# Performance work log

Hardware: AMD Instinct MI355X
Metric: run time of the kernel (lower is better)

## Reference

```python
import jax, jax.numpy as jnp
import numpy as np
from jax import lax

K = 9
CENTER = K // 2
EXTEND = 1.0
EPS = 1e-5
GROUPS = 16  # out_ch // 4


def conv2d(x, w, b, stride, padding):
    y = lax.conv_general_dilated(x, w, window_strides=stride, padding=padding,
                                 dimension_numbers=('NCHW', 'OIHW', 'NCHW'))
    return y + b[None, :, None, None]


def setup_inputs() -> dict:
    key = jax.random.key(0)
    ks = jax.random.split(key, 9)
    B, C, Wd, Hd, OUT = 8, 64, 128, 128, 64
    f = jax.random.normal(ks[0], (B, C, Wd, Hd), jnp.float32)
    w_off = jax.random.normal(ks[1], (2 * K, C, 3, 3), jnp.float32) * 0.05
    b_off = jax.random.normal(ks[2], (2 * K,), jnp.float32) * 0.05
    bn_gamma = 1.0 + 0.1 * jax.random.normal(ks[3], (2 * K,), jnp.float32)
    bn_beta = 0.1 * jax.random.normal(ks[4], (2 * K,), jnp.float32)
    w_dsc = jax.random.normal(ks[5], (OUT, C, K, 1), jnp.float32) * 0.05
    b_dsc = jax.random.normal(ks[6], (OUT,), jnp.float32) * 0.05
    gn_gamma = 1.0 + 0.1 * jax.random.normal(ks[7], (OUT,), jnp.float32)
    gn_beta = 0.1 * jax.random.normal(ks[8], (OUT,), jnp.float32)
    return {'f': f, 'w_off': w_off, 'b_off': b_off, 'bn_gamma': bn_gamma,
            'bn_beta': bn_beta, 'w_dsc': w_dsc, 'b_dsc': b_dsc,
            'gn_gamma': gn_gamma, 'gn_beta': gn_beta}


def _forward(f, w_off, b_off, bn_gamma, bn_beta, w_dsc, b_dsc, gn_gamma, gn_beta):
    B, C, Wd, Hd = f.shape  # module names: width=shape[2], height=shape[3]
    dt = f.dtype

    # offset branch: conv3x3 -> BatchNorm (training mode, batch stats) -> tanh
    off = conv2d(f, w_off, b_off, (1, 1), 'SAME')
    mu = off.mean(axis=(0, 2, 3), keepdims=True)
    var = off.var(axis=(0, 2, 3), keepdims=True)
    off = (off - mu) / jnp.sqrt(var + EPS)
    off = off * bn_gamma[None, :, None, None] + bn_beta[None, :, None, None]
    off = jnp.tanh(off)

    y_off = off[:, :K]  # [B,K,Wd,Hd]; x_off (off[:, K:]) unused for morph=0

    # cumulative offset scan from the center point (morph=0).
    # NOTE: endpoints 0 and K-1 keep detached raw offsets (torch detach().clone()).
    raw0 = lax.stop_gradient(y_off)
    offn = [None] * K
    offn[CENTER] = jnp.zeros_like(y_off[:, 0])
    for i in range(1, CENTER):
        offn[CENTER + i] = offn[CENTER + i - 1] + y_off[:, CENTER + i]
        offn[CENTER - i] = offn[CENTER - i + 1] + y_off[:, CENTER - i]
    offn[0] = raw0[:, 0]
    offn[K - 1] = raw0[:, K - 1]
    offn = jnp.stack(offn, axis=1)  # [B,K,Wd,Hd]

    # coordinate grids: y indexes the width axis, x the height axis
    y_new = jnp.arange(Wd, dtype=dt)[None, None, :, None] + offn * EXTEND  # [B,K,Wd,Hd]
    x_new = ((jnp.arange(K, dtype=dt) - CENTER)[None, :, None, None]
             + jnp.arange(Hd, dtype=dt)[None, None, None, :])  # [1,K,1,Hd]
    x_new = jnp.broadcast_to(x_new, (B, K, Wd, Hd))

    # layout [B, K*Wd, Hd] via (B,K,Wd,Hd) -> (B,Wd,K,Hd)
    y_s = jnp.transpose(y_new, (0, 2, 1, 3)).reshape(B, K * Wd * Hd)
    x_s = jnp.transpose(x_new, (0, 2, 1, 3)).reshape(B, K * Wd * Hd)

    # bilinear interpolation (clamped corner indices, unclamped y/x in weights)
    y0 = jnp.floor(y_s).astype(jnp.int32)
    x0 = jnp.floor(x_s).astype(jnp.int32)
    y0c = jnp.clip(y0, 0, Wd - 1)
    y1c = jnp.clip(y0 + 1, 0, Wd - 1)
    x0c = jnp.clip(x0, 0, Hd - 1)
    x1c = jnp.clip(x0 + 1, 0, Hd - 1)

    feat = jnp.transpose(f, (0, 2, 3, 1)).reshape(B, Wd * Hd, C)

    def gather(yi, xi):
        idx = (yi * Hd + xi)[:, :, None]  # [B,N,1]
        return jnp.take_along_axis(feat, idx, axis=1)  # [B,N,C]

    va0 = gather(y0c, x0c)
    vc0 = gather(y0c, x1c)
    va1 = gather(y1c, x0c)
    vc1 = gather(y1c, x1c)

    y0f, y1f = y0c.astype(dt), y1c.astype(dt)
    x0f, x1f = x0c.astype(dt), x1c.astype(dt)
    wa = ((y1f - y_s) * (x1f - x_s))[:, :, None]
    wb = ((y1f - y_s) * (x_s - x0f))[:, :, None]
    wc = ((y_s - y0f) * (x1f - x_s))[:, :, None]
    wd = ((y_s - y0f) * (x_s - x0f))[:, :, None]

    out = va0 * wa + vc0 * wb + va1 * wc + vc1 * wd  # [B,N,C]
    deformed = jnp.transpose(out.reshape(B, K * Wd, Hd, C), (0, 3, 1, 2))  # [B,C,K*Wd,Hd]

    # strided conv over the K snake points -> [B,OUT,Wd,Hd]
    x = conv2d(deformed, w_dsc, b_dsc, (K, 1), 'VALID')

    # GroupNorm + ReLU
    OUT = x.shape[1]
    xg = x.reshape(B, GROUPS, -1)
    gmu = xg.mean(axis=-1, keepdims=True)
    gvar = xg.var(axis=-1, keepdims=True)
    xg = (xg - gmu) / jnp.sqrt(gvar + EPS)
    x = xg.reshape(x.shape) * gn_gamma[None, :, None, None] + gn_beta[None, :, None, None]
    return jax.nn.relu(x)


def reference(f, w_off, b_off, bn_gamma, bn_beta, w_dsc, b_dsc, gn_gamma, gn_beta):
    return _forward(f, w_off, b_off, bn_gamma, bn_beta, w_dsc, b_dsc, gn_gamma, gn_beta)
```

## Files before the change

kernel.cpp:

```cpp
#include <hip/hip_runtime.h>

#define B_   8
#define C_   64
#define W_   128
#define H_   128
#define K_   9
#define OUT_ 64
#define NPIX (B_*W_*H_)
#define EPS_ 1e-5f

typedef __attribute__((ext_vector_type(8))) short bf16x8;
typedef __attribute__((ext_vector_type(4))) float f32x4;

#define FEATBF_OFF  0
#define XPRE_OFF    4194304
#define OFFPRE_OFF  8388608
#define OFFH_OFF    9568256
#define WT_OFF      14286848
#define WP_OFF      14305280
#define BNSTATS_OFF 14310464
#define BNAB_OFF    14310482
#define GSTATS_OFF  14310500
#define GNFIN_OFF   14310756
#define STATS_BYTES ((18+18+256+256)*sizeof(float))

__device__ __forceinline__ unsigned pack2bf(float a, float b) {
    union { float f; unsigned u; } ua, ub;
    ua.f = a; ub.f = b;
    unsigned x = ua.u, y = ub.u;
    x += 0x7fffu + ((x >> 16) & 1u);
    y += 0x7fffu + ((y >> 16) & 1u);
    return (x >> 16) | (y & 0xffff0000u);
}
__device__ __forceinline__ float bflo(unsigned u) {
    union { unsigned u; float f; } v; v.u = u << 16; return v.f;
}
__device__ __forceinline__ float bfhi(unsigned u) {
    union { unsigned u; float f; } v; v.u = u & 0xffff0000u; return v.f;
}

__global__ __launch_bounds__(256) void k_nhwc(const float* __restrict__ f,
                                              unsigned short* __restrict__ featbf) {
    __shared__ float tile[64][65];
    int bid = blockIdx.x;
    int ht = bid & 1;
    int w  = (bid >> 1) & 127;
    int b  = bid >> 8;
    int t  = threadIdx.x;
    int lh = t & 63;
    int c0 = (t >> 6) * 16;
    const float* fp = f + (((b*64)*128 + w)*128) + ht*64 + lh;
#pragma unroll
    for (int i = 0; i < 16; i++) {
        int c = c0 + i;
        tile[c][lh] = fp[c*16384];
    }
    __syncthreads();
    int lc = t & 63;
    int h0 = (t >> 6) * 16;
    unsigned short* obf = featbf + ((size_t)((b*128 + w)*128) + ht*64)*64 + lc;
#pragma unroll
    for (int i = 0; i < 16; i++) {
        int hr = h0 + i;
        union { float f; unsigned u; } v; v.f = tile[lc][hr];
        unsigned x = v.u + 0x7fffu + ((v.u >> 16) & 1u);
        obf[(size_t)hr*64] = (unsigned short)(x >> 16);
    }
}

__global__ void k_wt(const float* __restrict__ w_dsc, unsigned short* __restrict__ wTbf) {
    int i = blockIdx.x*256 + threadIdx.x;
    if (i >= 9*64*64) return;
    int c = i & 63;
    int o = (i >> 6) & 63;
    int k = i >> 12;
    union { float f; unsigned u; } v;
    v.f = w_dsc[(o*64 + c)*9 + k];
    unsigned x = v.u + 0x7fffu + ((v.u >> 16) & 1u);
    wTbf[i] = (unsigned short)(x >> 16);
}

__global__ void k_wp(const float* __restrict__ w_off, float* __restrict__ wP) {
    int i = blockIdx.x*256 + threadIdx.x;
    if (i >= 64*81) return;
    int c    = i / 81;
    int rem  = i % 81;
    int dw   = rem / 27;
    int rem2 = rem % 27;
    int ck   = rem2 / 3;
    int dh   = rem2 % 3;
    wP[i] = w_off[ck*576 + c*9 + dw*3 + dh];
}

__global__ __launch_bounds__(128) void k_conv_off(const float* __restrict__ f,
                                                  const float* __restrict__ wP,
                                                  float* __restrict__ off_half) {
    int t   = threadIdx.x;
    int bid = blockIdx.x;
    int b   = bid & 7;
    int w   = (bid >> 3) & 127;
    int cq  = bid >> 10;
    int h   = t;

    float em = (h == 0)   ? 0.f : 1.f;
    float ep = (h == 127) ? 0.f : 1.f;

    const float* fb = f + (size_t)b*1048576 + (size_t)(cq*16)*16384 + (size_t)w*128;
    const float* wb = wP + cq*16*81;

    float acc[9];
#pragma unroll
    for (int ck = 0; ck < 9; ck++) acc[ck] = 0.f;

#pragma unroll 4
    for (int c = 0; c < 16; c++) {
        const float* p  = fb + c*16384;
        const float* wc = wb + c*81;
#pragma unroll
        for (int dw = -1; dw <= 1; dw++) {
            int wy = w + dw;
            if ((unsigned)wy < 128u) {
                const float* q = p + dw*128;
                float v1 = q[h];
                float v0 = __shfl_up(v1, 1);
                float v2 = __shfl_down(v1, 1);
                if (t == 64) v0 = q[63];
                if (t == 63) v2 = q[64];
                v0 *= em; v2 *= ep;
                const float* ww = wc + (dw+1)*27;
#pragma unroll
                for (int ck = 0; ck < 9; ck++)
                    acc[ck] += v0*ww[ck*3] + v1*ww[ck*3+1] + v2*ww[ck*3+2];
            }
        }
    }

    float* dst = off_half + (size_t)cq*1179648;
    int pixoff = (w << 7) + h;
#pragma unroll
    for (int ck = 0; ck < 9; ck++)
        dst[((b*9 + ck) << 14) + pixoff] = acc[ck];
}

__global__ __launch_bounds__(256) void k_bn_stats(const float* __restrict__ off_half,
                                                  float* __restrict__ off_pre,
                                                  float* __restrict__ bnstats) {
    __shared__ float wred[4][2];
    int bid = blockIdx.x;
    int b  = bid / 36;
    int rem = bid % 36;
    int ck = rem / 4;
    int wq = rem % 4;
    int t  = threadIdx.x;
    int base4 = (((b*9+ck) << 14) + wq*4096) >> 2;

    const float4* h0 = (const float4*)off_half;
    const float4* h1 = (const float4*)(off_half + 1179648);
    const float4* h2 = (const float4*)(off_half + 2359296);
    const float4* h3 = (const float4*)(off_half + 3538944);
    float4* op = (float4*)off_pre;

    float s = 0.f, q = 0.f;
#pragma unroll
    for (int i = 0; i < 4; i++) {
        int idx = base4 + t + i*256;
        float4 a = h0[idx], bb = h1[idx], cc = h2[idx], dd = h3[idx];
        float4 v;
        v.x = (a.x + bb.x) + (cc.x + dd.x);
        v.y = (a.y + bb.y) + (cc.y + dd.y);
        v.z = (a.z + bb.z) + (cc.z + dd.z);
        v.w = (a.w + bb.w) + (cc.w + dd.w);
        op[idx] = v;
        s += v.x + v.y + v.z + v.w;
        q += v.x*v.x + v.y*v.y + v.z*v.z + v.w*v.w;
    }
    for (int off = 32; off; off >>= 1) {
        s += __shfl_down(s, off);
        q += __shfl_down(q, off);
    }
    if ((t & 63) == 0) { wred[t >> 6][0] = s; wred[t >> 6][1] = q; }
    __syncthreads();
    if (t == 0) atomicAdd(&bnstats[ck*2],   wred[0][0]+wred[1][0]+wred[2][0]+wred[3][0]);
    if (t == 1) atomicAdd(&bnstats[ck*2+1], wred[0][1]+wred[1][1]+wred[2][1]+wred[3][1]);
}

__global__ void k_bn_fin(const float* __restrict__ bnstats,
                         const float* __restrict__ bn_gamma,
                         const float* __restrict__ bn_beta,
                         float* __restrict__ bnAB) {
    int t = threadIdx.x;
    if (t < 9) {
        float n    = (float)NPIX;
        float mean = bnstats[t*2] / n;
        float var  = bnstats[t*2+1] / n - mean*mean;
        float A    = bn_gamma[t] / sqrtf(var + EPS_);
        bnAB[t*2]   = A;
        bnAB[t*2+1] = bn_beta[t] - mean * A;
    }
}

__global__ __launch_bounds__(256) void k_sample_dsc(const unsigned short* __restrict__ featbf,
                                                    const float* __restrict__ off_pre,
                                                    const float* __restrict__ bnAB,
                                                    const unsigned short* __restrict__ wTbf,
                                                    const float* __restrict__ b_dsc,
                                                    unsigned short* __restrict__ xprebf,
                                                    float* __restrict__ gstats) {
    __shared__ __align__(16) unsigned char lds_samp[128*128];
    __shared__ __align__(16) unsigned char lds_wk[64*128];
    __shared__ float ynew[9][128];
    __shared__ float red[16][2];

    int t = threadIdx.x;
    int b = blockIdx.x & 7, w = blockIdx.x >> 3;

    if (t < 128) {
        int h = t;
        float y[9];
#pragma unroll
        for (int ck = 0; ck < 9; ck++) {
            float v = off_pre[((b*9+ck) << 14) + (w << 7) + h];
            y[ck] = tanhf(bnAB[ck*2]*v + bnAB[ck*2+1]);
        }
        float ofn[9];
        ofn[4] = 0.f;
        ofn[5] = y[5]; ofn[6] = y[5]+y[6]; ofn[7] = y[5]+y[6]+y[7];
        ofn[3] = y[3]; ofn[2] = y[3]+y[2]; ofn[1] = y[3]+y[2]+y[1];
        ofn[0] = y[0]; ofn[8] = y[8];
#pragma unroll
        for (int k = 0; k < 9; k++) ynew[k][h] = (float)w + ofn[k];
    }
    if (t < 16) { red[t][0] = 0.f; red[t][1] = 0.f; }

    f32x4 acc[2][4];
#pragma unroll
    for (int mi = 0; mi < 2; mi++)
#pragma unroll
        for (int ni = 0; ni < 4; ni++) {
            acc[mi][ni][0] = 0.f; acc[mi][ni][1] = 0.f;
            acc[mi][ni][2] = 0.f; acc[mi][ni][3] = 0.f;
        }

    int lane = t & 63, wv = t >> 6;
    int m0 = wv * 32;
    int lm = lane & 15, lk = lane >> 4;
    int hs = t >> 1;
    int cq = (t & 1) * 4;

    __syncthreads();

    for (int k = 0; k < 9; k++) {
        if (k) __syncthreads();

        {
            const uint4* src = (const uint4*)(wTbf + (k << 12));
#pragma unroll
            for (int i = 0; i < 2; i++) {
                int ci = t + i*256;
                uint4 v = src[ci];
                int o  = ci >> 3;
                int cb = (ci & 7) << 4;
                *(uint4*)(lds_wk + o*128 + (cb ^ ((o & 7) << 4))) = v;
            }
        }

        {
            int x0 = k - 4 + hs;
            unsigned char* dst = lds_samp + hs*128;
            int bcol0 = (t & 1) * 64;
            if ((unsigned)x0 < 127u) {
                float ys = ynew[k][hs];
                int y0  = (int)floorf(ys);
                int y0c = min(max(y0, 0), 127), y1c = min(max(y0+1, 0), 127);
                float wa = (float)y1c - ys;
                float wc = ys - (float)y0c;
                const unsigned short* pb = featbf + ((size_t)b << 20);
                const uint4* p0 = (const uint4*)(pb + (y0c*128 + x0)*64) + cq;
                const uint4* p1 = (const uint4*)(pb + (y1c*128 + x0)*64) + cq;
#pragma unroll
                for (int ci = 0; ci < 4; ci++) {
                    uint4 a = p0[ci], c = p1[ci];
                    uint4 u;
                    u.x = pack2bf(bflo(a.x)*wa + bflo(c.x)*wc, bfhi(a.x)*wa + bfhi(c.x)*wc);
                    u.y = pack2bf(bflo(a.y)*wa + bflo(c.y)*wc, bfhi(a.y)*wa + bfhi(c.y)*wc);
                    u.z = pack2bf(bflo(a.z)*wa + bflo(c.z)*wc, bfhi(a.z)*wa + bfhi(c.z)*wc);
                    u.w = pack2bf(bflo(a.w)*wa + bflo(c.w)*wc, bfhi(a.w)*wa + bfhi(c.w)*wc);
                    *(uint4*)(dst + ((bcol0 + ci*16) ^ ((hs & 7) << 4))) = u;
                }
            } else {
                uint4 z = make_uint4(0,0,0,0);
#pragma unroll
                for (int ci = 0; ci < 4; ci++)
                    *(uint4*)(dst + ((bcol0 + ci*16) ^ ((hs & 7) << 4))) = z;
            }
        }
        __syncthreads();

#pragma unroll
        for (int ks = 0; ks < 2; ks++) {
            bf16x8 af[2], bfr[4];
#pragma unroll
            for (int mi = 0; mi < 2; mi++) {
                int h = m0 + mi*16 + lm;
                af[mi] = *(const bf16x8*)(lds_samp + h*128 + ((ks*64 + lk*16) ^ ((h & 7) << 4)));
            }
#pragma unroll
            for (int ni = 0; ni < 4; ni++) {
                int o = ni*16 + lm;
                bfr[ni] = *(const bf16x8*)(lds_wk + o*128 + ((ks*64 + lk*16) ^ ((o & 7) << 4)));
            }
#pragma unroll
            for (int mi = 0; mi < 2; mi++)
#pragma unroll
                for (int ni = 0; ni < 4; ni++)
                    acc[mi][ni] = __builtin_amdgcn_mfma_f32_16x16x32_bf16(af[mi], bfr[ni], acc[mi][ni], 0, 0, 0);
        }
    }

#pragma unroll
    for (int ni = 0; ni < 4; ni++) {
        int o = ni*16 + lm;
        float bias = b_dsc[o];
        float s1 = 0.f, s2 = 0.f;
#pragma unroll
        for (int mi = 0; mi < 2; mi++) {
            float4 r;
            r.x = acc[mi][ni][0] + bias;
            r.y = acc[mi][ni][1] + bias;
            r.z = acc[mi][ni][2] + bias;
            r.w = acc[mi][ni][3] + bias;
            s1 += r.x + r.y + r.z + r.w;
            s2 += r.x*r.x + r.y*r.y + r.z*r.z + r.w*r.w;
            int h = m0 + mi*16 + lk*4;
            uint2 u2;
            u2.x = pack2bf(r.x, r.y);
            u2.y = pack2bf(r.z, r.w);
            *(uint2*)(xprebf + (((b*64 + o) << 14) + (w << 7) + h)) = u2;
        }
        s1 += __shfl_xor(s1, 1);  s1 += __shfl_xor(s1, 2);
        s1 += __shfl_xor(s1, 16); s1 += __shfl_xor(s1, 32);
        s2 += __shfl_xor(s2, 1);  s2 += __shfl_xor(s2, 2);
        s2 += __shfl_xor(s2, 16); s2 += __shfl_xor(s2, 32);
        if (lk == 0 && (lm & 3) == 0) {
            atomicAdd(&red[ni*4 + (lm >> 2)][0], s1);
            atomicAdd(&red[ni*4 + (lm >> 2)][1], s2);
        }
    }
    __syncthreads();
    if (t < 16) {
        atomicAdd(&gstats[(b*16 + t)*2],   red[t][0]);
        atomicAdd(&gstats[(b*16 + t)*2+1], red[t][1]);
    }
}

__global__ void k_gn_fin(const float* __restrict__ gstats, float* __restrict__ gnfin) {
    int t = threadIdx.x;
    if (t < 128) {
        float n    = 65536.f;
        float mean = gstats[t*2] / n;
        float var  = gstats[t*2+1] / n - mean*mean;
        gnfin[t*2]   = mean;
        gnfin[t*2+1] = 1.0f / sqrtf(var + EPS_);
    }
}

__global__ __launch_bounds__(256) void k_gn_apply(const unsigned short* __restrict__ xprebf,
                                                  const float* __restrict__ gnfin,
                                                  const float* __restrict__ gn_gamma,
                                                  const float* __restrict__ gn_beta,
                                                  float* __restrict__ out) {
    int i8  = blockIdx.x*256 + threadIdx.x;
    int idx = i8 * 8;
    int o = (idx >> 14) & 63;
    int b = idx >> 20;
    int g = o >> 2;
    float mean = gnfin[(b*16+g)*2];
    float istd = gnfin[(b*16+g)*2+1];
    float ga = gn_gamma[o] * istd;
    float be = gn_beta[o] - mean * ga;
    uint4 v = *(const uint4*)(xprebf + idx);
    float4 r0, r1;
    r0.x = fmaxf(bflo(v.x)*ga + be, 0.f);
    r0.y = fmaxf(bfhi(v.x)*ga + be, 0.f);
    r0.z = fmaxf(bflo(v.y)*ga + be, 0.f);
    r0.w = fmaxf(bfhi(v.y)*ga + be, 0.f);
    r1.x = fmaxf(bflo(v.z)*ga + be, 0.f);
    r1.y = fmaxf(bfhi(v.z)*ga + be, 0.f);
    r1.z = fmaxf(bflo(v.w)*ga + be, 0.f);
    r1.w = fmaxf(bfhi(v.w)*ga + be, 0.f);
    *(float4*)(out + idx)     = r0;
    *(float4*)(out + idx + 4) = r1;
}

extern "C" void kernel_launch(void* const* d_in, const int* in_sizes, int n_in,
                              void* d_out, int out_size, void* d_ws, size_t ws_size,
                              hipStream_t stream) {
    const float* f        = (const float*)d_in[0];
    const float* w_off    = (const float*)d_in[1];
    const float* bn_gamma = (const float*)d_in[3];
    const float* bn_beta  = (const float*)d_in[4];
    const float* w_dsc    = (const float*)d_in[5];
    const float* b_dsc    = (const float*)d_in[6];
    const float* gn_gamma = (const float*)d_in[7];
    const float* gn_beta  = (const float*)d_in[8];

    float* ws      = (float*)d_ws;
    unsigned short* featbf = (unsigned short*)(ws + FEATBF_OFF);
    unsigned short* xprebf = (unsigned short*)(ws + XPRE_OFF);
    float* off_pre = ws + OFFPRE_OFF;
    float* off_half= ws + OFFH_OFF;
    unsigned short* wTbf = (unsigned short*)(ws + WT_OFF);
    float* wP      = ws + WP_OFF;
    float* bnstats = ws + BNSTATS_OFF;
    float* bnAB    = ws + BNAB_OFF;
    float* gstats  = ws + GSTATS_OFF;
    float* gnfin   = ws + GNFIN_OFF;

    hipMemsetAsync(bnstats, 0, STATS_BYTES, stream);

    k_nhwc<<<2048, 256, 0, stream>>>(f, featbf);
    k_wt<<<144, 256, 0, stream>>>(w_dsc, wTbf);
    k_wp<<<21, 256, 0, stream>>>(w_off, wP);
    k_conv_off<<<4096, 128, 0, stream>>>(f, wP, off_half);
    k_bn_stats<<<288, 256, 0, stream>>>(off_half, off_pre, bnstats);
    k_bn_fin<<<1, 32, 0, stream>>>(bnstats, bn_gamma, bn_beta, bnAB);
    k_sample_dsc<<<1024, 256, 0, stream>>>(featbf, off_pre, bnAB, wTbf, b_dsc, xprebf, gstats);
    k_gn_fin<<<1, 128, 0, stream>>>(gstats, gnfin);
    k_gn_apply<<<4096, 256, 0, stream>>>(xprebf, gnfin, gn_gamma, gn_beta, (float*)d_out);
}
```

Measured before the change: 123.0 us.

## Register-tile offset conv over four rows and split channels into eight partials

The offset conv kernel now computes four adjacent output rows per block, loading six input rows once per channel and reusing them across the 3x3 window. It also replaces the shuffle-based neighbour exchange with direct indexed loads. Channels are split into eight groups of eight instead of four groups of sixteen, so the BN-stats kernel now sums eight partial buffers and the workspace grows. The aim is to cut redundant input loads, at the cost of more accumulator registers and more partial-sum traffic.

```diff
diff --git a/kernel.cpp b/kernel.cpp
--- a/kernel.cpp
+++ b/kernel.cpp
@@ -16,12 +16,12 @@
 #define XPRE_OFF    4194304
 #define OFFPRE_OFF  8388608
 #define OFFH_OFF    9568256
-#define WT_OFF      14286848
-#define WP_OFF      14305280
-#define BNSTATS_OFF 14310464
-#define BNAB_OFF    14310482
-#define GSTATS_OFF  14310500
-#define GNFIN_OFF   14310756
+#define WT_OFF      19005440
+#define WP_OFF      19023872
+#define BNSTATS_OFF 19029056
+#define BNAB_OFF    19029074
+#define GSTATS_OFF  19029092
+#define GNFIN_OFF   19029348
 #define STATS_BYTES ((18+18+256+256)*sizeof(float))
 
 __device__ __forceinline__ unsigned pack2bf(float a, float b) {
@@ -98,48 +98,60 @@
     int t   = threadIdx.x;
     int bid = blockIdx.x;
     int b   = bid & 7;
-    int w   = (bid >> 3) & 127;
-    int cq  = bid >> 10;
+    int ws  = (bid >> 3) & 31;
+    int cq  = bid >> 8;
+    int w0  = ws * 4;
     int h   = t;
 
     float em = (h == 0)   ? 0.f : 1.f;
     float ep = (h == 127) ? 0.f : 1.f;
-
-    const float* fb = f + (size_t)b*1048576 + (size_t)(cq*16)*16384 + (size_t)w*128;
-    const float* wb = wP + cq*16*81;
-
-    float acc[9];
-#pragma unroll
-    for (int ck = 0; ck < 9; ck++) acc[ck] = 0.f;
-
-#pragma unroll 4
-    for (int c = 0; c < 16; c++) {
+    int   om = h + ((h == 0)   ? 0 : -1);
+    int   op = h + ((h == 127) ? 0 : 1);
+
+    const float* fb = f + (size_t)b*1048576 + (size_t)(cq*8)*16384;
+    const float* wb = wP + cq*8*81;
+
+    float acc[4][9];
+#pragma unroll
+    for (int wi = 0; wi < 4; wi++)
+#pragma unroll
+        for (int ck = 0; ck < 9; ck++) acc[wi][ck] = 0.f;
+
+#pragma unroll 2
+    for (int c = 0; c < 8; c++) {
         const float* p  = fb + c*16384;
         const float* wc = wb + c*81;
-#pragma unroll
-        for (int dw = -1; dw <= 1; dw++) {
-            int wy = w + dw;
-            if ((unsigned)wy < 128u) {
-                const float* q = p + dw*128;
-                float v1 = q[h];
-                float v0 = __shfl_up(v1, 1);
-                float v2 = __shfl_down(v1, 1);
-                if (t == 64) v0 = q[63];
-                if (t == 63) v2 = q[64];
-                v0 *= em; v2 *= ep;
-                const float* ww = wc + (dw+1)*27;
+        float t0[6], t1[6], t2[6];
+#pragma unroll
+        for (int r = 0; r < 6; r++) {
+            int wy = w0 - 1 + r;
+            float mv = ((unsigned)wy < 128u) ? 1.f : 0.f;
+            const float* q = p + (((unsigned)wy < 128u) ? wy : 0)*128;
+            t0[r] = q[om] * (em * mv);
+            t1[r] = q[h]  * mv;
+            t2[r] = q[op] * (ep * mv);
+        }
+#pragma unroll
+        for (int dw = 0; dw < 3; dw++) {
+            const float* ww = wc + dw*27;
+#pragma unroll
+            for (int wi = 0; wi < 4; wi++) {
+                int r = wi + dw;
 #pragma unroll
                 for (int ck = 0; ck < 9; ck++)
-                    acc[ck] += v0*ww[ck*3] + v1*ww[ck*3+1] + v2*ww[ck*3+2];
+                    acc[wi][ck] += t0[r]*ww[ck*3] + t1[r]*ww[ck*3+1] + t2[r]*ww[ck*3+2];
             }
         }
     }
 
     float* dst = off_half + (size_t)cq*1179648;
-    int pixoff = (w << 7) + h;
-#pragma unroll
-    for (int ck = 0; ck < 9; ck++)
-        dst[((b*9 + ck) << 14) + pixoff] = acc[ck];
+#pragma unroll
+    for (int wi = 0; wi < 4; wi++) {
+        int pixoff = ((w0 + wi) << 7) + h;
+#pragma unroll
+        for (int ck = 0; ck < 9; ck++)
+            dst[((b*9 + ck) << 14) + pixoff] = acc[wi][ck];
+    }
 }
 
 __global__ __launch_bounds__(256) void k_bn_stats(const float* __restrict__ off_half,
@@ -154,22 +166,18 @@
     int t  = threadIdx.x;
     int base4 = (((b*9+ck) << 14) + wq*4096) >> 2;
 
-    const float4* h0 = (const float4*)off_half;
-    const float4* h1 = (const float4*)(off_half + 1179648);
-    const float4* h2 = (const float4*)(off_half + 2359296);
-    const float4* h3 = (const float4*)(off_half + 3538944);
+    float s = 0.f, q = 0.f;
     float4* op = (float4*)off_pre;
-
-    float s = 0.f, q = 0.f;
 #pragma unroll
     for (int i = 0; i < 4; i++) {
         int idx = base4 + t + i*256;
-        float4 a = h0[idx], bb = h1[idx], cc = h2[idx], dd = h3[idx];
-        float4 v;
-        v.x = (a.x + bb.x) + (cc.x + dd.x);
-        v.y = (a.y + bb.y) + (cc.y + dd.y);
-        v.z = (a.z + bb.z) + (cc.z + dd.z);
-        v.w = (a.w + bb.w) + (cc.w + dd.w);
+        float4 v = make_float4(0.f, 0.f, 0.f, 0.f);
+#pragma unroll
+        for (int pp = 0; pp < 8; pp++) {
+            const float4* hp = (const float4*)(off_half + (size_t)pp*1179648);
+            float4 a = hp[idx];
+            v.x += a.x; v.y += a.y; v.z += a.z; v.w += a.w;
+        }
         op[idx] = v;
         s += v.x + v.y + v.z + v.w;
         q += v.x*v.x + v.y*v.y + v.z*v.z + v.w*v.w;
@@ -421,7 +429,7 @@
     k_nhwc<<<2048, 256, 0, stream>>>(f, featbf);
     k_wt<<<144, 256, 0, stream>>>(w_dsc, wTbf);
     k_wp<<<21, 256, 0, stream>>>(w_off, wP);
-    k_conv_off<<<4096, 128, 0, stream>>>(f, wP, off_half);
+    k_conv_off<<<2048, 128, 0, stream>>>(f, wP, off_half);
     k_bn_stats<<<288, 256, 0, stream>>>(off_half, off_pre, bnstats);
     k_bn_fin<<<1, 32, 0, stream>>>(bnstats, bn_gamma, bn_beta, bnAB);
     k_sample_dsc<<<1024, 256, 0, stream>>>(featbf, off_pre, bnAB, wTbf, b_dsc, xprebf, gstats);
```

New measurement: 131.3 us. +6.7%, slower.

## Fold tiny finalize kernels into consumers and prefetch DSC weights across iterations

Applied to the files above, without the earlier changes.

Merges the two weight-prep kernels into one launch, and removes the BN and GN finalize kernels by recomputing their statistics inside k_sample_dsc and k_gn_apply. It also prefetches the next tap's weight tile into registers before the barrier so the global load overlaps the MMA step. This cuts three kernel launches and their serialization gaps, at the cost of redundant per-block finalize math and extra registers in the sampling kernel.

```diff
diff --git a/kernel.cpp b/kernel.cpp
--- a/kernel.cpp
+++ b/kernel.cpp
@@ -19,9 +19,7 @@
 #define WT_OFF      14286848
 #define WP_OFF      14305280
 #define BNSTATS_OFF 14310464
-#define BNAB_OFF    14310482
 #define GSTATS_OFF  14310500
-#define GNFIN_OFF   14310756
 #define STATS_BYTES ((18+18+256+256)*sizeof(float))
 
 __device__ __forceinline__ unsigned pack2bf(float a, float b) {
@@ -68,28 +66,30 @@
     }
 }
 
-__global__ void k_wt(const float* __restrict__ w_dsc, unsigned short* __restrict__ wTbf) {
-    int i = blockIdx.x*256 + threadIdx.x;
-    if (i >= 9*64*64) return;
-    int c = i & 63;
-    int o = (i >> 6) & 63;
-    int k = i >> 12;
-    union { float f; unsigned u; } v;
-    v.f = w_dsc[(o*64 + c)*9 + k];
-    unsigned x = v.u + 0x7fffu + ((v.u >> 16) & 1u);
-    wTbf[i] = (unsigned short)(x >> 16);
-}
-
-__global__ void k_wp(const float* __restrict__ w_off, float* __restrict__ wP) {
-    int i = blockIdx.x*256 + threadIdx.x;
-    if (i >= 64*81) return;
-    int c    = i / 81;
-    int rem  = i % 81;
-    int dw   = rem / 27;
-    int rem2 = rem % 27;
-    int ck   = rem2 / 3;
-    int dh   = rem2 % 3;
-    wP[i] = w_off[ck*576 + c*9 + dw*3 + dh];
+__global__ void k_wprep(const float* __restrict__ w_dsc, unsigned short* __restrict__ wTbf,
+                        const float* __restrict__ w_off, float* __restrict__ wP) {
+    int bid = blockIdx.x;
+    if (bid < 144) {
+        int i = bid*256 + threadIdx.x;
+        if (i >= 9*64*64) return;
+        int c = i & 63;
+        int o = (i >> 6) & 63;
+        int k = i >> 12;
+        union { float f; unsigned u; } v;
+        v.f = w_dsc[(o*64 + c)*9 + k];
+        unsigned x = v.u + 0x7fffu + ((v.u >> 16) & 1u);
+        wTbf[i] = (unsigned short)(x >> 16);
+    } else {
+        int i = (bid-144)*256 + threadIdx.x;
+        if (i >= 64*81) return;
+        int c    = i / 81;
+        int rem  = i % 81;
+        int dw   = rem / 27;
+        int rem2 = rem % 27;
+        int ck   = rem2 / 3;
+        int dh   = rem2 % 3;
+        wP[i] = w_off[ck*576 + c*9 + dw*3 + dh];
+    }
 }
 
 __global__ __launch_bounds__(128) void k_conv_off(const float* __restrict__ f,
@@ -184,24 +184,11 @@
     if (t == 1) atomicAdd(&bnstats[ck*2+1], wred[0][1]+wred[1][1]+wred[2][1]+wred[3][1]);
 }
 
-__global__ void k_bn_fin(const float* __restrict__ bnstats,
-                         const float* __restrict__ bn_gamma,
-                         const float* __restrict__ bn_beta,
-                         float* __restrict__ bnAB) {
-    int t = threadIdx.x;
-    if (t < 9) {
-        float n    = (float)NPIX;
-        float mean = bnstats[t*2] / n;
-        float var  = bnstats[t*2+1] / n - mean*mean;
-        float A    = bn_gamma[t] / sqrtf(var + EPS_);
-        bnAB[t*2]   = A;
-        bnAB[t*2+1] = bn_beta[t] - mean * A;
-    }
-}
-
 __global__ __launch_bounds__(256) void k_sample_dsc(const unsigned short* __restrict__ featbf,
                                                     const float* __restrict__ off_pre,
-                                                    const float* __restrict__ bnAB,
+                                                    const float* __restrict__ bnstats,
+                                                    const float* __restrict__ bn_gamma,
+                                                    const float* __restrict__ bn_beta,
                                                     const unsigned short* __restrict__ wTbf,
                                                     const float* __restrict__ b_dsc,
                                                     unsigned short* __restrict__ xprebf,
@@ -210,9 +197,21 @@
     __shared__ __align__(16) unsigned char lds_wk[64*128];
     __shared__ float ynew[9][128];
     __shared__ float red[16][2];
+    __shared__ float bnab[18];
 
     int t = threadIdx.x;
     int b = blockIdx.x & 7, w = blockIdx.x >> 3;
+
+    if (t < 9) {
+        float n    = (float)NPIX;
+        float mean = bnstats[t*2] / n;
+        float var  = bnstats[t*2+1] / n - mean*mean;
+        float A    = bn_gamma[t] / sqrtf(var + EPS_);
+        bnab[t*2]   = A;
+        bnab[t*2+1] = bn_beta[t] - mean * A;
+    }
+    if (t < 16) { red[t][0] = 0.f; red[t][1] = 0.f; }
+    __syncthreads();
 
     if (t < 128) {
         int h = t;
@@ -220,7 +219,7 @@
 #pragma unroll
         for (int ck = 0; ck < 9; ck++) {
             float v = off_pre[((b*9+ck) << 14) + (w << 7) + h];
-            y[ck] = tanhf(bnAB[ck*2]*v + bnAB[ck*2+1]);
+            y[ck] = tanhf(bnab[ck*2]*v + bnab[ck*2+1]);
         }
         float ofn[9];
         ofn[4] = 0.f;
@@ -230,7 +229,6 @@
 #pragma unroll
         for (int k = 0; k < 9; k++) ynew[k][h] = (float)w + ofn[k];
     }
-    if (t < 16) { red[t][0] = 0.f; red[t][1] = 0.f; }
 
     f32x4 acc[2][4];
 #pragma unroll
@@ -247,17 +245,23 @@
     int hs = t >> 1;
     int cq = (t & 1) * 4;
 
+    uint4 wv0, wv1;
+    {
+        const uint4* src = (const uint4*)wTbf;
+        wv0 = src[t];
+        wv1 = src[t + 256];
+    }
+
     __syncthreads();
 
     for (int k = 0; k < 9; k++) {
         if (k) __syncthreads();
 
         {
-            const uint4* src = (const uint4*)(wTbf + (k << 12));
 #pragma unroll
             for (int i = 0; i < 2; i++) {
                 int ci = t + i*256;
-                uint4 v = src[ci];
+                uint4 v = (i == 0) ? wv0 : wv1;
                 int o  = ci >> 3;
                 int cb = (ci & 7) << 4;
                 *(uint4*)(lds_wk + o*128 + (cb ^ ((o & 7) << 4))) = v;
@@ -294,6 +298,12 @@
                     *(uint4*)(dst + ((bcol0 + ci*16) ^ ((hs & 7) << 4))) = z;
             }
         }
+
+        if (k < 8) {
+            const uint4* src = (const uint4*)(wTbf + ((k+1) << 12));
+            wv0 = src[t];
+            wv1 = src[t + 256];
+        }
         __syncthreads();
 
 #pragma unroll
@@ -353,19 +363,8 @@
     }
 }
 
-__global__ void k_gn_fin(const float* __restrict__ gstats, float* __restrict__ gnfin) {
-    int t = threadIdx.x;
-    if (t < 128) {
-        float n    = 65536.f;
-        float mean = gstats[t*2] / n;
-        float var  = gstats[t*2+1] / n - mean*mean;
-        gnfin[t*2]   = mean;
-        gnfin[t*2+1] = 1.0f / sqrtf(var + EPS_);
-    }
-}
-
 __global__ __launch_bounds__(256) void k_gn_apply(const unsigned short* __restrict__ xprebf,
-                                                  const float* __restrict__ gnfin,
+                                                  const float* __restrict__ gstats,
                                                   const float* __restrict__ gn_gamma,
                                                   const float* __restrict__ gn_beta,
                                                   float* __restrict__ out) {
@@ -374,8 +373,10 @@
     int o = (idx >> 14) & 63;
     int b = idx >> 20;
     int g = o >> 2;
-    float mean = gnfin[(b*16+g)*2];
-    float istd = gnfin[(b*16+g)*2+1];
+    float n    = 65536.f;
+    float mean = gstats[(b*16+g)*2] / n;
+    float var  = gstats[(b*16+g)*2+1] / n - mean*mean;
+    float istd = 1.0f / sqrtf(var + EPS_);
     float ga = gn_gamma[o] * istd;
     float be = gn_beta[o] - mean * ga;
     uint4 v = *(const uint4*)(xprebf + idx);
@@ -412,19 +413,15 @@
     unsigned short* wTbf = (unsigned short*)(ws + WT_OFF);
     float* wP      = ws + WP_OFF;
     float* bnstats = ws + BNSTATS_OFF;
-    float* bnAB    = ws + BNAB_OFF;
     float* gstats  = ws + GSTATS_OFF;
-    float* gnfin   = ws + GNFIN_OFF;
 
     hipMemsetAsync(bnstats, 0, STATS_BYTES, stream);
 
     k_nhwc<<<2048, 256, 0, stream>>>(f, featbf);
-    k_wt<<<144, 256, 0, stream>>>(w_dsc, wTbf);
-    k_wp<<<21, 256, 0, stream>>>(w_off, wP);
+    k_wprep<<<165, 256, 0, stream>>>(w_dsc, wTbf, w_off, wP);
     k_conv_off<<<4096, 128, 0, stream>>>(f, wP, off_half);
     k_bn_stats<<<288, 256, 0, stream>>>(off_half, off_pre, bnstats);
-    k_bn_fin<<<1, 32, 0, stream>>>(bnstats, bn_gamma, bn_beta, bnAB);
-    k_sample_dsc<<<1024, 256, 0, stream>>>(featbf, off_pre, bnAB, wTbf, b_dsc, xprebf, gstats);
-    k_gn_fin<<<1, 128, 0, stream>>>(gstats, gnfin);
-    k_gn_apply<<<4096, 256, 0, stream>>>(xprebf, gnfin, gn_gamma, gn_beta, (float*)d_out);
-}
+    k_sample_dsc<<<1024, 256, 0, stream>>>(featbf, off_pre, bnstats, bn_gamma, bn_beta,
+                                           wTbf, b_dsc, xprebf, gstats);
+    k_gn_apply<<<4096, 256, 0, stream>>>(xprebf, gstats, gn_gamma, gn_beta, (float*)d_out);
+}
```

New measurement: 126.3 us. +2.7%, slower.
